# Optimization experiments

Hardware: AMD Instinct MI355X
Metric: run time of the kernel (lower is better)

## Reference

```python
import jax, jax.numpy as jnp
import numpy as np
from jax import lax

B, S, DM = 4, 4096, 1024
H, P, R = 16, 32, 8
D = DM // H  # head_dim = 64
K_SEL = 4


def setup_inputs() -> dict:
    key = jax.random.key(0)
    ks = jax.random.split(key, 6)
    x = jax.random.normal(ks[0], (B, S, DM), dtype=jnp.float32)
    K_state = jax.random.normal(ks[1], (H, P, R, D), dtype=jnp.float32) / np.sqrt(D)
    V_state = jax.random.normal(ks[2], (H, P, R, D), dtype=jnp.float32) / np.sqrt(D)
    W_router = jax.random.normal(ks[3], (H, D, P), dtype=jnp.float32) / np.sqrt(D)
    W_out = jax.random.normal(ks[4], (DM, DM), dtype=jnp.float32) / np.sqrt(DM)
    b_out = jnp.zeros((DM,), dtype=jnp.float32)
    return {"x": x, "K_state": K_state, "V_state": V_state,
            "W_router": W_router, "W_out": W_out, "b_out": b_out, "k": K_SEL}


def reference(x, K_state, V_state, W_router, W_out, b_out, k):
    b, s, dm = x.shape
    h, p, r, d = K_state.shape
    xh = x.reshape(b, s, h, d)  # per-head token features

    # Router: top-k partition selection per token per head.
    logits = jnp.einsum('bshd,hdp->bshp', xh, W_router)
    topv = lax.top_k(logits, k)[0]            # [b,s,h,k]
    thresh = topv[..., -1:]                   # k-th largest logit
    neg_inf = jnp.array(-jnp.inf, dtype=logits.dtype)
    gates = jax.nn.softmax(jnp.where(logits >= thresh, logits, neg_inf), axis=-1)  # [b,s,h,p], zero off top-k

    # Attention over state rows within each partition (masked-dense == sparse gather math).
    scale = jnp.asarray(1.0 / np.sqrt(d), dtype=x.dtype)
    scores = jnp.einsum('bshd,hprd->bshpr', xh, K_state) * scale
    attn = jax.nn.softmax(scores, axis=-1)    # softmax over rows r within a partition

    # Gate-weighted combine of per-partition attention outputs, fused to avoid [b,s,h,p,d].
    w = attn * gates[..., None]               # [b,s,h,p,r]
    heads = jnp.einsum('bshpr,hprd->bshd', w, V_state)

    out = heads.reshape(b, s, dm) @ W_out + b_out
    return out
```

## Files before the change

kernel.cpp:

```cpp
#include <hip/hip_runtime.h>
#include <hip/hip_bf16.h>

#define BB 4
#define SS 4096
#define DM 1024
#define HH 16
#define PP 32
#define RR 8
#define DD 64
#define NTOK (BB*SS)
#define MM NTOK
#define NN DM
#define KK DM

typedef __attribute__((ext_vector_type(8))) short short8;
typedef __attribute__((ext_vector_type(4))) float floatx4;

static __device__ inline short f2bf(float f) {
    union { __hip_bfloat16 b; short s; } u; u.b = __float2bfloat16(f); return u.s;
}
static __device__ inline short8 pack8(float4 lo, float4 hi) {
    short8 r;
    r[0] = f2bf(lo.x); r[1] = f2bf(lo.y); r[2] = f2bf(lo.z); r[3] = f2bf(lo.w);
    r[4] = f2bf(hi.x); r[5] = f2bf(hi.y); r[6] = f2bf(hi.z); r[7] = f2bf(hi.w);
    return r;
}

static __device__ inline unsigned bfr(float f) {
    unsigned u = __float_as_uint(f);
    return u + 0x7fffu + ((u >> 16) & 1u);
}
static __device__ inline int pk2(float a, float b) {
    return __builtin_amdgcn_perm(bfr(b), bfr(a), 0x07060302);
}
static __device__ inline short8 pk8(float4 lo, float4 hi) {
    union { short8 s; int i[4]; } r;
    r.i[0] = pk2(lo.x, lo.y); r.i[1] = pk2(lo.z, lo.w);
    r.i[2] = pk2(hi.x, hi.y); r.i[3] = pk2(hi.z, hi.w);
    return r.s;
}

__global__ __launch_bounds__(256) void convert_w(const float* __restrict__ Wo,
                                                 __hip_bfloat16* __restrict__ wsw) {
    int tid = blockIdx.x * 256 + threadIdx.x;
    int l = tid & 63;
    int kblk = (tid >> 6) & 31;
    int ntile = tid >> 11;
    int col = ntile * 16 + (l & 15);
    int krow = kblk * 32 + (l >> 4) * 8;
#pragma unroll
    for (int j = 0; j < 8; ++j) {
        wsw[(size_t)tid * 8 + j] = __float2bfloat16(Wo[(size_t)(krow + j) * NN + col]);
    }
}

__global__ __launch_bounds__(256) void convert_kv(const float* __restrict__ Kst,
                                                  const float* __restrict__ Vst,
                                                  __hip_bfloat16* __restrict__ kfrag,
                                                  __hip_bfloat16* __restrict__ vfrag) {
    int tid = blockIdx.x * 256 + threadIdx.x;
    int arr = tid >> 15;
    int idx = tid & 32767;
    int h = idx >> 11, blk = (idx >> 6) & 31, fl = idx & 63;
    int fm = fl & 15, fk = fl >> 4;
    short8 val;
    short* dst;
    if (arr == 0) {
        int mt = blk >> 1, kb = blk & 1;
        int pr = mt * 16 + fm, d0 = kb * 32 + fk * 8;
        const float* src = Kst + ((size_t)h * 256 + pr) * 64 + d0;
        float4 lo = *(const float4*)src, hi = *(const float4*)(src + 4);
        val = pack8(lo, hi);
        dst = (short*)kfrag + (size_t)idx * 8;
    } else {
        int mt = blk >> 3, kb = blk & 7;
        int d = mt * 16 + fm, pr0 = kb * 32 + fk * 8;
        const float* src = Vst + ((size_t)h * 256 + pr0) * 64 + d;
#pragma unroll
        for (int j = 0; j < 8; ++j) val[j] = f2bf(src[j * 64]);
        dst = (short*)vfrag + (size_t)idx * 8;
    }
    *(short8*)dst = val;
}

__global__ __launch_bounds__(256, 3) void attn_v4(const float* __restrict__ x,
                                                  const float* __restrict__ Wr,
                                                  const __hip_bfloat16* __restrict__ kfrag,
                                                  const __hip_bfloat16* __restrict__ vfrag,
                                                  const int* __restrict__ kp,
                                                  __hip_bfloat16* __restrict__ hb) {
    __shared__ __align__(16) char smem[41984];
    float (*xs)[68]    = (float (*)[68])smem;
    float (*Lg)[36]    = (float (*)[36])(smem + 17408);
    short* wf          = (short*)smem;
    float (*gates)[36] = (float (*)[36])(smem + 32768);

    const int lane = threadIdx.x & 63;
    const int w = threadIdx.x >> 6;
    const int l15 = lane & 15, l4 = lane >> 4;
    const int t0 = blockIdx.x * 64;
    const int h = blockIdx.y;

    {
        int row = threadIdx.x >> 2, q = threadIdx.x & 3;
        const float4* src = (const float4*)(x + (size_t)(t0 + row) * DM + h * 64 + q * 16);
        float4 v0 = src[0], v1 = src[1], v2 = src[2], v3 = src[3];
        float4* dst = (float4*)&xs[row][q * 16];
        dst[0] = v0; dst[1] = v1; dst[2] = v2; dst[3] = v3;
    }

    const int p = lane & 31, dh = lane >> 5;
    float wreg[32];
    {
        const float* wrp = Wr + (size_t)h * (DD * PP) + dh * 32 * PP + p;
#pragma unroll
        for (int dd = 0; dd < 32; ++dd) wreg[dd] = wrp[dd * PP];
    }
    const int kkv = kp[0];

    __syncthreads();

    short8 xb[4][2];
#pragma unroll
    for (int nt = 0; nt < 4; ++nt)
#pragma unroll
        for (int kb = 0; kb < 2; ++kb) {
            const float* bp = x + (size_t)(t0 + nt * 16 + l15) * DM + h * 64 + kb * 32 + l4 * 8;
            float4 lo = *(const float4*)bp;
            float4 hi = *(const float4*)(bp + 4);
            xb[nt][kb] = pk8(lo, hi);
        }
    short8 ka[4][2];
#pragma unroll
    for (int mi = 0; mi < 4; ++mi)
#pragma unroll
        for (int kb = 0; kb < 2; ++kb)
            ka[mi][kb] = *(const short8*)((const short*)kfrag +
                          ((size_t)(h * 32 + (w * 4 + mi) * 2 + kb) * 512 + lane * 8));

    floatx4 acc[4][4] = {};
#pragma unroll
    for (int kb = 0; kb < 2; ++kb)
#pragma unroll
        for (int mi = 0; mi < 4; ++mi)
#pragma unroll
            for (int nt = 0; nt < 4; ++nt)
                acc[mi][nt] = __builtin_amdgcn_mfma_f32_16x16x32_bf16(ka[mi][kb], xb[nt][kb], acc[mi][nt], 0, 0, 0);

    for (int it = 0; it < 16; ++it) {
        int t = w * 16 + it;
        float xf[32];
#pragma unroll
        for (int j = 0; j < 8; ++j) {
            float4 tq = *(const float4*)&xs[t][dh * 32 + 4 * j];
            xf[4 * j] = tq.x; xf[4 * j + 1] = tq.y; xf[4 * j + 2] = tq.z; xf[4 * j + 3] = tq.w;
        }
        float lg = 0.f;
#pragma unroll
        for (int dd = 0; dd < 32; ++dd) lg += xf[dd] * wreg[dd];
        lg += __shfl_xor(lg, 32);
        if (lane < 32) Lg[t][lane] = lg;
    }
    __syncthreads();

    if (lane < 16) {
        int t = w * 16 + lane;
        float lgr[32];
        const float4* lrow = (const float4*)&Lg[t][0];
#pragma unroll
        for (int c = 0; c < 8; ++c) {
            float4 q4 = lrow[c];
            lgr[4 * c] = q4.x; lgr[4 * c + 1] = q4.y; lgr[4 * c + 2] = q4.z; lgr[4 * c + 3] = q4.w;
        }
        float a1 = -INFINITY, b2 = -INFINITY, c3 = -INFINITY, d4 = -INFINITY;
#pragma unroll
        for (int pp = 0; pp < 32; ++pp) {
            float v = lgr[pp];
            float na = fmaxf(a1, v); v = fminf(a1, v); a1 = na;
            float nb = fmaxf(b2, v); v = fminf(b2, v); b2 = nb;
            float nc = fmaxf(c3, v); v = fminf(c3, v); c3 = nc;
            d4 = fmaxf(d4, v);
        }
        float thresh = (kkv >= 4) ? d4 : (kkv == 3 ? c3 : (kkv == 2 ? b2 : a1));
        float den = 0.f;
        float garr[32];
#pragma unroll
        for (int pp = 0; pp < 32; ++pp) {
            float e = __expf(lgr[pp] - a1);
            float ge = (lgr[pp] >= thresh) ? e : 0.f;
            garr[pp] = ge; den += ge;
        }
        float inv = 1.f / den;
        float4* grow = (float4*)&gates[t][0];
#pragma unroll
        for (int c = 0; c < 8; ++c)
            grow[c] = make_float4(garr[4 * c] * inv, garr[4 * c + 1] * inv,
                                  garr[4 * c + 2] * inv, garr[4 * c + 3] * inv);
    }
    __syncthreads();

#pragma unroll
    for (int mi = 0; mi < 4; ++mi) {
        const int mt = w * 4 + mi;
        const int pidx = mt * 2 + (l4 >> 1);
#pragma unroll
        for (int nt = 0; nt < 4; ++nt) {
            float g = gates[nt * 16 + l15][pidx];
            float s0 = acc[mi][nt][0] * 0.125f;
            float s1 = acc[mi][nt][1] * 0.125f;
            float s2 = acc[mi][nt][2] * 0.125f;
            float s3 = acc[mi][nt][3] * 0.125f;
            float mx = fmaxf(fmaxf(s0, s1), fmaxf(s2, s3));
            mx = fmaxf(mx, __shfl_xor(mx, 16));
            float e0 = __expf(s0 - mx), e1 = __expf(s1 - mx);
            float e2 = __expf(s2 - mx), e3 = __expf(s3 - mx);
            float loc = (e0 + e1) + (e2 + e3);
            float se = loc + __shfl_xor(loc, 16);
            float ws = g / se;
            int2 pk;
            pk.x = pk2(e0 * ws, e1 * ws);
            pk.y = pk2(e2 * ws, e3 * ws);
            int off = (((mt & 1) * 2 + (l4 >> 1)) * 16 + l15) * 8 + (l4 & 1) * 4;
            *(int2*)&wf[(nt * 8 + (mt >> 1)) * 512 + off] = pk;
        }
    }
    __syncthreads();

    floatx4 h4[4] = {};
#pragma unroll
    for (int kb = 0; kb < 8; ++kb) {
        short8 va = *(const short8*)((const short*)vfrag +
                      ((size_t)(h * 32 + w * 8 + kb) * 512 + lane * 8));
#pragma unroll
        for (int nt = 0; nt < 4; ++nt) {
            short8 wb = *(const short8*)&wf[(nt * 8 + kb) * 512 + lane * 8];
            h4[nt] = __builtin_amdgcn_mfma_f32_16x16x32_bf16(va, wb, h4[nt], 0, 0, 0);
        }
    }
#pragma unroll
    for (int nt = 0; nt < 4; ++nt) {
        int t = t0 + nt * 16 + l15;
        int2 pk;
        pk.x = pk2(h4[nt][0], h4[nt][1]);
        pk.y = pk2(h4[nt][2], h4[nt][3]);
        *(int2*)((short*)hb + (size_t)t * DM + h * 64 + w * 16 + l4 * 4) = pk;
    }
}

__global__ __launch_bounds__(256) void gemm_v2(const __hip_bfloat16* __restrict__ Abf,
                                               const __hip_bfloat16* __restrict__ Bsw,
                                               const float* __restrict__ bias,
                                               float* __restrict__ C) {
    __shared__ __align__(16) short As[4096];
    const int lane = threadIdx.x & 63;
    const int wave = threadIdx.x >> 6;
    const int wm = wave >> 1, wn = wave & 1;
    const int bm0 = blockIdx.y * 128;
    const int bn0 = blockIdx.x * 128;
    const int l15 = lane & 15, l4 = lane >> 4;

    const short* Ap = (const short*)Abf;
    const short* Bp = (const short*)Bsw;

    const int c0 = (wave * 2 + 0) * 64 + lane;
    const int c1 = (wave * 2 + 1) * 64 + lane;
    const short* g0 = Ap + (size_t)(bm0 + (c0 >> 2)) * KK + (c0 & 3) * 8;
    const short* g1 = Ap + (size_t)(bm0 + (c1 >> 2)) * KK + (c1 & 3) * 8;
    short* l0 = &As[(wave * 2 + 0) * 512];
    short* l1 = &As[(wave * 2 + 1) * 512];

    int boff[4];
#pragma unroll
    for (int nt = 0; nt < 4; ++nt)
        boff[nt] = (((bn0 >> 4) + wn * 4 + nt) * 32) * 512 + lane * 8;

    int aoff[4];
#pragma unroll
    for (int mt = 0; mt < 4; ++mt)
        aoff[mt] = ((wm * 64 + mt * 16 + l15) * 4 + l4) * 8;

    floatx4 acc[4][4] = {};

    for (int kb = 0; kb < 32; ++kb) {
        __syncthreads();
        short8 b[4];
#pragma unroll
        for (int nt = 0; nt < 4; ++nt)
            b[nt] = *(const short8*)(Bp + boff[nt] + kb * 512);
        __builtin_amdgcn_global_load_lds(
            (const __attribute__((address_space(1))) unsigned int*)(g0 + kb * 32),
            (__attribute__((address_space(3))) unsigned int*)l0, 16, 0, 0);
        __builtin_amdgcn_global_load_lds(
            (const __attribute__((address_space(1))) unsigned int*)(g1 + kb * 32),
            (__attribute__((address_space(3))) unsigned int*)l1, 16, 0, 0);
        __syncthreads();
        short8 a[4];
#pragma unroll
        for (int mt = 0; mt < 4; ++mt)
            a[mt] = *(const short8*)&As[aoff[mt]];
#pragma unroll
        for (int mt = 0; mt < 4; ++mt)
#pragma unroll
            for (int nt = 0; nt < 4; ++nt)
                acc[mt][nt] = __builtin_amdgcn_mfma_f32_16x16x32_bf16(a[mt], b[nt], acc[mt][nt], 0, 0, 0);
    }

#pragma unroll
    for (int nt = 0; nt < 4; ++nt) {
        const int col = bn0 + wn * 64 + nt * 16 + l15;
        const float bv = bias[col];
#pragma unroll
        for (int mt = 0; mt < 4; ++mt) {
            const int row0 = bm0 + wm * 64 + mt * 16 + l4 * 4;
#pragma unroll
            for (int i = 0; i < 4; ++i)
                C[(size_t)(row0 + i) * NN + col] = acc[mt][nt][i] + bv;
        }
    }
}

extern "C" void kernel_launch(void* const* d_in, const int* in_sizes, int n_in,
                              void* d_out, int out_size, void* d_ws, size_t ws_size,
                              hipStream_t stream) {
    const float* x   = (const float*)d_in[0];
    const float* Kst = (const float*)d_in[1];
    const float* Vst = (const float*)d_in[2];
    const float* Wr  = (const float*)d_in[3];
    const float* Wo  = (const float*)d_in[4];
    const float* bo  = (const float*)d_in[5];
    const int*   kp  = (const int*)d_in[6];
    float* out = (float*)d_out;

    __hip_bfloat16* hb    = (__hip_bfloat16*)d_ws;
    __hip_bfloat16* wsw   = hb + (size_t)MM * KK;
    __hip_bfloat16* kfrag = wsw + (size_t)KK * NN;
    __hip_bfloat16* vfrag = kfrag + 16 * 32 * 512;

    convert_w<<<dim3(512), 256, 0, stream>>>(Wo, wsw);
    convert_kv<<<dim3(256), 256, 0, stream>>>(Kst, Vst, kfrag, vfrag);
    attn_v4<<<dim3(NTOK / 64, HH), 256, 0, stream>>>(x, Wr, kfrag, vfrag, kp, hb);
    gemm_v2<<<dim3(NN / 128, MM / 128), 256, 0, stream>>>(hb, wsw, bo, out);
}
```

Baseline: 267.0 us.

## Double-buffer GEMM A tiles, swizzle blocks per XCD, and transpose gate storage

The output GEMM now double-buffers the A tile in LDS and prefetches the next B fragments into registers, cutting one barrier per k-step so loads overlap the MFMAs. Workgroups are remapped so each of the 8 XCDs gets a contiguous band of M rows, aiming for better L2 reuse. The attention kernel stores gates transposed ([p][t]), trims shared memory, and raises launch bounds to 4 blocks per SM for occupancy. The costs are more registers and LDS in the GEMM, and possible register spills in attention at the tighter occupancy bound.

```diff
diff --git a/kernel.cpp b/kernel.cpp
--- a/kernel.cpp
+++ b/kernel.cpp
@@ -83,17 +83,17 @@
     *(short8*)dst = val;
 }
 
-__global__ __launch_bounds__(256, 3) void attn_v4(const float* __restrict__ x,
+__global__ __launch_bounds__(256, 4) void attn_v5(const float* __restrict__ x,
                                                   const float* __restrict__ Wr,
                                                   const __hip_bfloat16* __restrict__ kfrag,
                                                   const __hip_bfloat16* __restrict__ vfrag,
                                                   const int* __restrict__ kp,
                                                   __hip_bfloat16* __restrict__ hb) {
-    __shared__ __align__(16) char smem[41984];
-    float (*xs)[68]    = (float (*)[68])smem;
-    float (*Lg)[36]    = (float (*)[36])(smem + 17408);
-    short* wf          = (short*)smem;
-    float (*gates)[36] = (float (*)[36])(smem + 32768);
+    __shared__ __align__(16) char smem[40960];
+    float (*xs)[68]     = (float (*)[68])smem;
+    float (*Lg)[36]     = (float (*)[36])(smem + 17408);
+    short* wf           = (short*)smem;
+    float (*gatesT)[64] = (float (*)[64])(smem + 32768);
 
     const int lane = threadIdx.x & 63;
     const int w = threadIdx.x >> 6;
@@ -191,11 +191,9 @@
             garr[pp] = ge; den += ge;
         }
         float inv = 1.f / den;
-        float4* grow = (float4*)&gates[t][0];
-#pragma unroll
-        for (int c = 0; c < 8; ++c)
-            grow[c] = make_float4(garr[4 * c] * inv, garr[4 * c + 1] * inv,
-                                  garr[4 * c + 2] * inv, garr[4 * c + 3] * inv);
+#pragma unroll
+        for (int pp = 0; pp < 32; ++pp)
+            gatesT[pp][t] = garr[pp] * inv;
     }
     __syncthreads();
 
@@ -205,7 +203,7 @@
         const int pidx = mt * 2 + (l4 >> 1);
 #pragma unroll
         for (int nt = 0; nt < 4; ++nt) {
-            float g = gates[nt * 16 + l15][pidx];
+            float g = gatesT[pidx][nt * 16 + l15];
             float s0 = acc[mi][nt][0] * 0.125f;
             float s1 = acc[mi][nt][1] * 0.125f;
             float s2 = acc[mi][nt][2] * 0.125f;
@@ -247,16 +245,21 @@
     }
 }
 
-__global__ __launch_bounds__(256) void gemm_v2(const __hip_bfloat16* __restrict__ Abf,
+__global__ __launch_bounds__(256) void gemm_v3(const __hip_bfloat16* __restrict__ Abf,
                                                const __hip_bfloat16* __restrict__ Bsw,
                                                const float* __restrict__ bias,
                                                float* __restrict__ C) {
-    __shared__ __align__(16) short As[4096];
+    __shared__ __align__(16) short As[2][4096];
     const int lane = threadIdx.x & 63;
     const int wave = threadIdx.x >> 6;
     const int wm = wave >> 1, wn = wave & 1;
-    const int bm0 = blockIdx.y * 128;
-    const int bn0 = blockIdx.x * 128;
+
+    const int wg  = blockIdx.y * 8 + blockIdx.x;
+    const int xcd = wg & 7;
+    const int loc = wg >> 3;
+    const int bm0 = (xcd * 16 + (loc >> 3)) * 128;
+    const int bn0 = (loc & 7) * 128;
+
     const int l15 = lane & 15, l4 = lane >> 4;
 
     const short* Ap = (const short*)Abf;
@@ -266,8 +269,6 @@
     const int c1 = (wave * 2 + 1) * 64 + lane;
     const short* g0 = Ap + (size_t)(bm0 + (c0 >> 2)) * KK + (c0 & 3) * 8;
     const short* g1 = Ap + (size_t)(bm0 + (c1 >> 2)) * KK + (c1 & 3) * 8;
-    short* l0 = &As[(wave * 2 + 0) * 512];
-    short* l1 = &As[(wave * 2 + 1) * 512];
 
     int boff[4];
 #pragma unroll
@@ -281,28 +282,45 @@
 
     floatx4 acc[4][4] = {};
 
+    __builtin_amdgcn_global_load_lds(
+        (const __attribute__((address_space(1))) unsigned int*)(g0),
+        (__attribute__((address_space(3))) unsigned int*)&As[0][(wave * 2 + 0) * 512], 16, 0, 0);
+    __builtin_amdgcn_global_load_lds(
+        (const __attribute__((address_space(1))) unsigned int*)(g1),
+        (__attribute__((address_space(3))) unsigned int*)&As[0][(wave * 2 + 1) * 512], 16, 0, 0);
+    short8 bcur[4], bnxt[4];
+#pragma unroll
+    for (int nt = 0; nt < 4; ++nt)
+        bcur[nt] = *(const short8*)(Bp + boff[nt]);
+    __syncthreads();
+
     for (int kb = 0; kb < 32; ++kb) {
+        const int cur = kb & 1;
+        const int nxt = cur ^ 1;
+        if (kb < 31) {
+            __builtin_amdgcn_global_load_lds(
+                (const __attribute__((address_space(1))) unsigned int*)(g0 + (kb + 1) * 32),
+                (__attribute__((address_space(3))) unsigned int*)&As[nxt][(wave * 2 + 0) * 512], 16, 0, 0);
+            __builtin_amdgcn_global_load_lds(
+                (const __attribute__((address_space(1))) unsigned int*)(g1 + (kb + 1) * 32),
+                (__attribute__((address_space(3))) unsigned int*)&As[nxt][(wave * 2 + 1) * 512], 16, 0, 0);
+#pragma unroll
+            for (int nt = 0; nt < 4; ++nt)
+                bnxt[nt] = *(const short8*)(Bp + boff[nt] + (kb + 1) * 512);
+        }
+        short8 a[4];
+#pragma unroll
+        for (int mt = 0; mt < 4; ++mt)
+            a[mt] = *(const short8*)&As[cur][aoff[mt]];
+#pragma unroll
+        for (int mt = 0; mt < 4; ++mt)
+#pragma unroll
+            for (int nt = 0; nt < 4; ++nt)
+                acc[mt][nt] = __builtin_amdgcn_mfma_f32_16x16x32_bf16(a[mt], bcur[nt], acc[mt][nt], 0, 0, 0);
         __syncthreads();
-        short8 b[4];
 #pragma unroll
         for (int nt = 0; nt < 4; ++nt)
-            b[nt] = *(const short8*)(Bp + boff[nt] + kb * 512);
-        __builtin_amdgcn_global_load_lds(
-            (const __attribute__((address_space(1))) unsigned int*)(g0 + kb * 32),
-            (__attribute__((address_space(3))) unsigned int*)l0, 16, 0, 0);
-        __builtin_amdgcn_global_load_lds(
-            (const __attribute__((address_space(1))) unsigned int*)(g1 + kb * 32),
-            (__attribute__((address_space(3))) unsigned int*)l1, 16, 0, 0);
-        __syncthreads();
-        short8 a[4];
-#pragma unroll
-        for (int mt = 0; mt < 4; ++mt)
-            a[mt] = *(const short8*)&As[aoff[mt]];
-#pragma unroll
-        for (int mt = 0; mt < 4; ++mt)
-#pragma unroll
-            for (int nt = 0; nt < 4; ++nt)
-                acc[mt][nt] = __builtin_amdgcn_mfma_f32_16x16x32_bf16(a[mt], b[nt], acc[mt][nt], 0, 0, 0);
+            bcur[nt] = bnxt[nt];
     }
 
 #pragma unroll
@@ -338,6 +356,6 @@
 
     convert_w<<<dim3(512), 256, 0, stream>>>(Wo, wsw);
     convert_kv<<<dim3(256), 256, 0, stream>>>(Kst, Vst, kfrag, vfrag);
-    attn_v4<<<dim3(NTOK / 64, HH), 256, 0, stream>>>(x, Wr, kfrag, vfrag, kp, hb);
-    gemm_v2<<<dim3(NN / 128, MM / 128), 256, 0, stream>>>(hb, wsw, bo, out);
-}
+    attn_v5<<<dim3(NTOK / 64, HH), 256, 0, stream>>>(x, Wr, kfrag, vfrag, kp, hb);
+    gemm_v3<<<dim3(NN / 128, MM / 128), 256, 0, stream>>>(hb, wsw, bo, out);
+}
```

Measured after the change: 323.2 us. 21.1% more time.
